# Kernel optimization log

Measured on AMD Instinct MI355X. Metric: run time of the kernel, lower is better.

## Reference

```python
import jax, jax.numpy as jnp
import numpy as np

O, I = 4096, 4096          # out_features, in_features
BLK = 32                   # GGML block size
NB = I // BLK              # blocks per output row
R = 16                     # LoRA rank
B, S = 8, 2048             # batch, seq
LORA_SCALE = 0.5           # alpha / rank
Q_ZERO = 128.0             # unsigned int storage -> signed via offset


def setup_inputs() -> dict:
    key = jax.random.key(0)
    k1, k2, k3, k4, k5, k6 = jax.random.split(key, 6)
    qweight = jax.random.randint(k1, (O, NB, BLK), 0, 256, dtype=jnp.int32)
    scales = jax.random.uniform(k2, (O, NB), dtype=jnp.float32) * 0.01
    lora_up = jax.random.normal(k3, (O, R), dtype=jnp.float32) * 0.02
    lora_down = jax.random.normal(k4, (R, I), dtype=jnp.float32) * 0.02
    bias = jax.random.normal(k5, (O,), dtype=jnp.float32)
    x = jax.random.normal(k6, (B, S, I), dtype=jnp.float32)
    return {"qweight": qweight, "scales": scales, "lora_up": lora_up,
            "lora_down": lora_down, "bias": bias, "x": x}


def reference(qweight, scales, lora_up, lora_down, bias, x):
    # GGML block dequantization: per-block scale times signed quantized values.
    deq = (scales[:, :, None] * (qweight.astype(jnp.float32) - Q_ZERO)).reshape(O, I)
    # LoRA-style patch applied to the dequantized weight.
    w = deq + LORA_SCALE * (lora_up @ lora_down)  # [O, I]
    # Fused use of the patched weight: linear layer.
    return jnp.einsum('bsi,oi->bso', x, w) + bias
```

## Files before the change

kernel.cpp:

```cpp
#include <hip/hip_runtime.h>
#include <stdint.h>

#define O_DIM 4096
#define I_DIM 4096
#define NB_DIM 128
#define R_DIM 16
#define M_DIM 16384
#define LORA_SCALE 0.5f
#define Q_ZERO 128.0f

typedef short bf16x8 __attribute__((ext_vector_type(8)));
typedef float f32x4 __attribute__((ext_vector_type(4)));

__device__ __forceinline__ uint16_t f2bf(float f) {
    union { float f; uint32_t u; } v; v.f = f;
    uint32_t u = v.u;
    return (uint16_t)((u + 0x7fffu + ((u >> 16) & 1u)) >> 16);
}

__device__ __forceinline__ void gll16(const void* g, void* l) {
    __builtin_amdgcn_global_load_lds(
        (const __attribute__((address_space(1))) void*)g,
        (__attribute__((address_space(3))) void*)l, 16, 0, 0);
}

__global__ void build_w_kernel(const int* __restrict__ qw,
                               const float* __restrict__ scales,
                               const float* __restrict__ up,
                               const float* __restrict__ down,
                               uint16_t* __restrict__ wout) {
    int idx = blockIdx.x * 256 + threadIdx.x;
    int i4  = idx & (I_DIM / 4 - 1);
    int o   = idx >> 10;
    int4 q = ((const int4*)qw)[(size_t)o * (I_DIM / 4) + i4];
    float scale = scales[o * NB_DIM + (i4 >> 3)];
    float a0 = 0.f, a1 = 0.f, a2 = 0.f, a3 = 0.f;
#pragma unroll
    for (int r = 0; r < R_DIM; ++r) {
        float u = up[o * R_DIM + r];
        float4 d = ((const float4*)down)[r * (I_DIM / 4) + i4];
        a0 += u * d.x; a1 += u * d.y; a2 += u * d.z; a3 += u * d.w;
    }
    float w0 = scale * ((float)q.x - Q_ZERO) + LORA_SCALE * a0;
    float w1 = scale * ((float)q.y - Q_ZERO) + LORA_SCALE * a1;
    float w2 = scale * ((float)q.z - Q_ZERO) + LORA_SCALE * a2;
    float w3 = scale * ((float)q.w - Q_ZERO) + LORA_SCALE * a3;
    ushort4 outv = { f2bf(w0), f2bf(w1), f2bf(w2), f2bf(w3) };
    ((ushort4*)wout)[(size_t)o * (I_DIM / 4) + i4] = outv;
}

__global__ void cvt_x_kernel(const float* __restrict__ x,
                             uint16_t* __restrict__ xb) {
    size_t idx = (size_t)blockIdx.x * 256 + threadIdx.x;
    float4 a = ((const float4*)x)[idx * 2];
    float4 b = ((const float4*)x)[idx * 2 + 1];
    ushort4 o0 = { f2bf(a.x), f2bf(a.y), f2bf(a.z), f2bf(a.w) };
    ushort4 o1 = { f2bf(b.x), f2bf(b.y), f2bf(b.z), f2bf(b.w) };
    ((ushort4*)xb)[idx * 2] = o0;
    ((ushort4*)xb)[idx * 2 + 1] = o1;
}

template <bool A_BF16>
__global__ void gemm_kernel(const uint16_t* __restrict__ Ab,
                            const float* __restrict__ Af,
                            const uint16_t* __restrict__ Wb,
                            const float* __restrict__ bias,
                            float* __restrict__ out) {
    __shared__ __align__(16) uint16_t As[128 * 32];
    __shared__ __align__(16) uint16_t Bs[128 * 32];
    const int tid = threadIdx.x;
    const int wave = tid >> 6, lane = tid & 63;
    const int m0 = blockIdx.y * 128;
    const int n0 = blockIdx.x * 128;
    const int wr = wave >> 1, wc = wave & 1;

    f32x4 acc[4][4] = {};

    const int lrow = lane & 15;
    const int lk = (lane >> 4) * 8;

    for (int k0 = 0; k0 < I_DIM; k0 += 32) {
        if (A_BF16) {
#pragma unroll
            for (int j = 0; j < 2; ++j) {
                int slot = wave * 2 + j;
                int row = slot * 16 + (lane >> 2);
                int col = (lane & 3) * 8;
                gll16(Ab + (size_t)(m0 + row) * I_DIM + k0 + col,
                      As + slot * 512);
            }
        } else {
            int row = tid >> 1;
            int col0 = (tid & 1) * 16;
            const float4* gp =
                (const float4*)(Af + (size_t)(m0 + row) * I_DIM + k0 + col0);
            float4 v0 = gp[0], v1 = gp[1], v2 = gp[2], v3 = gp[3];
            ushort4* dst = (ushort4*)&As[row * 32 + col0];
            ushort4 s0 = { f2bf(v0.x), f2bf(v0.y), f2bf(v0.z), f2bf(v0.w) };
            ushort4 s1 = { f2bf(v1.x), f2bf(v1.y), f2bf(v1.z), f2bf(v1.w) };
            ushort4 s2 = { f2bf(v2.x), f2bf(v2.y), f2bf(v2.z), f2bf(v2.w) };
            ushort4 s3 = { f2bf(v3.x), f2bf(v3.y), f2bf(v3.z), f2bf(v3.w) };
            dst[0] = s0; dst[1] = s1; dst[2] = s2; dst[3] = s3;
        }
#pragma unroll
        for (int j = 0; j < 2; ++j) {
            int slot = wave * 2 + j;
            int row = slot * 16 + (lane >> 2);
            int col = (lane & 3) * 8;
            gll16(Wb + (size_t)(n0 + row) * I_DIM + k0 + col,
                  Bs + slot * 512);
        }
        __syncthreads();

        bf16x8 a[4], b[4];
#pragma unroll
        for (int mi = 0; mi < 4; ++mi)
            a[mi] = *(const bf16x8*)&As[(wr * 64 + mi * 16 + lrow) * 32 + lk];
#pragma unroll
        for (int ni = 0; ni < 4; ++ni)
            b[ni] = *(const bf16x8*)&Bs[(wc * 64 + ni * 16 + lrow) * 32 + lk];
#pragma unroll
        for (int mi = 0; mi < 4; ++mi)
#pragma unroll
            for (int ni = 0; ni < 4; ++ni)
                acc[mi][ni] = __builtin_amdgcn_mfma_f32_16x16x32_bf16(
                    a[mi], b[ni], acc[mi][ni], 0, 0, 0);
        __syncthreads();
    }

    const int lcol = lane & 15;
    const int lquad = lane >> 4;
#pragma unroll
    for (int ni = 0; ni < 4; ++ni) {
        int n = n0 + wc * 64 + ni * 16 + lcol;
        float bv = bias[n];
#pragma unroll
        for (int mi = 0; mi < 4; ++mi) {
            int mbase = m0 + wr * 64 + mi * 16 + lquad * 4;
#pragma unroll
            for (int r = 0; r < 4; ++r)
                out[(size_t)(mbase + r) * O_DIM + n] = acc[mi][ni][r] + bv;
        }
    }
}

extern "C" void kernel_launch(void* const* d_in, const int* in_sizes, int n_in,
                              void* d_out, int out_size, void* d_ws,
                              size_t ws_size, hipStream_t stream) {
    const int* qweight = (const int*)d_in[0];
    const float* scales = (const float*)d_in[1];
    const float* lora_up = (const float*)d_in[2];
    const float* lora_down = (const float*)d_in[3];
    const float* bias = (const float*)d_in[4];
    const float* x = (const float*)d_in[5];
    float* out = (float*)d_out;

    uint16_t* w_bf16 = (uint16_t*)d_ws;
    const size_t w_bytes = (size_t)O_DIM * I_DIM * 2;
    uint16_t* x_bf16 = (uint16_t*)((char*)d_ws + w_bytes);
    const size_t need_full = w_bytes + (size_t)M_DIM * I_DIM * 2;

    build_w_kernel<<<O_DIM * I_DIM / 4 / 256, 256, 0, stream>>>(
        qweight, scales, lora_up, lora_down, w_bf16);

    dim3 grid(O_DIM / 128, M_DIM / 128);
    if (ws_size >= need_full) {
        cvt_x_kernel<<<(size_t)M_DIM * I_DIM / 8 / 256, 256, 0, stream>>>(
            x, x_bf16);
        gemm_kernel<true><<<grid, 256, 0, stream>>>(
            x_bf16, nullptr, w_bf16, bias, out);
    } else {
        gemm_kernel<false><<<grid, 256, 0, stream>>>(
            nullptr, x, w_bf16, bias, out);
    }
}
```

Baseline: 1.135 ms.

## Replace bf16 GEMM with 256x256-tile pipelined kernel using swizzled LDS and prefetch

Replaces the 128x128, single-buffered bf16 GEMM with a 512-thread kernel that computes 256x256 output tiles over K-steps of 64. LDS is double-buffered through direct global-to-LDS loads, with the next tiles' stages interleaved between MFMA groups and wait counts tuned for prefetch. LDS columns are XOR-swizzled to avoid bank conflicts, s_setprio is raised around the MFMA groups, and block IDs are remapped for L2 locality. The aim is more operand reuse per tile, overlap of loads with compute, and fewer stalls. The costs are 128KB of LDS per block, higher register pressure from 128 accumulators, and many barriers per iteration.

```diff
diff --git a/kernel.cpp b/kernel.cpp
--- a/kernel.cpp
+++ b/kernel.cpp
@@ -6,6 +6,7 @@
 #define NB_DIM 128
 #define R_DIM 16
 #define M_DIM 16384
+#define NT_K 64
 #define LORA_SCALE 0.5f
 #define Q_ZERO 128.0f
 
@@ -60,12 +61,10 @@
     ((ushort4*)xb)[idx * 2 + 1] = o1;
 }
 
-template <bool A_BF16>
-__global__ void gemm_kernel(const uint16_t* __restrict__ Ab,
-                            const float* __restrict__ Af,
-                            const uint16_t* __restrict__ Wb,
-                            const float* __restrict__ bias,
-                            float* __restrict__ out) {
+__global__ void gemm_kernel_f32a(const float* __restrict__ Af,
+                                 const uint16_t* __restrict__ Wb,
+                                 const float* __restrict__ bias,
+                                 float* __restrict__ out) {
     __shared__ __align__(16) uint16_t As[128 * 32];
     __shared__ __align__(16) uint16_t Bs[128 * 32];
     const int tid = threadIdx.x;
@@ -75,21 +74,11 @@
     const int wr = wave >> 1, wc = wave & 1;
 
     f32x4 acc[4][4] = {};
-
     const int lrow = lane & 15;
     const int lk = (lane >> 4) * 8;
 
     for (int k0 = 0; k0 < I_DIM; k0 += 32) {
-        if (A_BF16) {
-#pragma unroll
-            for (int j = 0; j < 2; ++j) {
-                int slot = wave * 2 + j;
-                int row = slot * 16 + (lane >> 2);
-                int col = (lane & 3) * 8;
-                gll16(Ab + (size_t)(m0 + row) * I_DIM + k0 + col,
-                      As + slot * 512);
-            }
-        } else {
+        {
             int row = tid >> 1;
             int col0 = (tid & 1) * 16;
             const float4* gp =
@@ -111,7 +100,6 @@
                   Bs + slot * 512);
         }
         __syncthreads();
-
         bf16x8 a[4], b[4];
 #pragma unroll
         for (int mi = 0; mi < 4; ++mi)
@@ -142,6 +130,140 @@
                 out[(size_t)(mbase + r) * O_DIM + n] = acc[mi][ni][r] + bv;
         }
     }
+}
+
+__global__ __launch_bounds__(512, 2)
+void gemm256_kernel(const uint16_t* __restrict__ Ab,
+                    const uint16_t* __restrict__ Wb,
+                    const float* __restrict__ bias,
+                    float* __restrict__ out) {
+    __shared__ __align__(16) char smem[131072];
+    const int tid = threadIdx.x;
+    const int wave = tid >> 6;
+    const int lane = tid & 63;
+
+    int bid = blockIdx.x;
+    int swz = (bid & 7) * 128 + (bid >> 3);
+    const int tn = swz >> 6;
+    const int tm = swz & 63;
+    const int m0 = tm * 256;
+    const int n0 = tn * 256;
+
+    const int wr = wave >> 2;
+    const int wc = wave & 3;
+
+    const int srow = lane >> 3;
+    const int sslot = (lane & 7) ^ srow;
+
+    const int l15 = lane & 15, q = lane >> 4, l7 = lane & 7;
+    const int ps0 = ((q ^ l7) << 4);
+    const int ps1 = (((4 | q) ^ l7) << 4);
+    const int abase = wr * 16384 + l15 * 128;
+    const int bbase = 65536 + (wc >> 1) * 16384 + ((wc & 1) * 64 + l15) * 128;
+
+    f32x4 acc[8][4] = {};
+    bf16x8 a[8][2], b[2][2];
+
+#define STAGE_HALF(mat, row0, kt, ldsb)                                       \
+    {                                                                         \
+        _Pragma("unroll")                                                     \
+        for (int j = 0; j < 2; ++j) {                                         \
+            const uint16_t* g = (mat) +                                       \
+                (size_t)((row0) + j * 64 + wave * 8 + srow) * I_DIM +         \
+                (size_t)(kt) * 64 + sslot * 8;                                \
+            gll16(g, smem + (ldsb) + (j * 64 + wave * 8) * 128);              \
+        }                                                                     \
+    }
+
+#define LDA(co, mi) do {                                                      \
+        a[mi][0] = *(const bf16x8*)(smem + (co) + abase + (mi) * 2048 + ps0); \
+        a[mi][1] = *(const bf16x8*)(smem + (co) + abase + (mi) * 2048 + ps1); \
+    } while (0)
+
+#define LDB(co, bi, nn) do {                                                  \
+        b[bi][0] = *(const bf16x8*)(smem + (co) + bbase + (nn) * 2048 + ps0); \
+        b[bi][1] = *(const bf16x8*)(smem + (co) + bbase + (nn) * 2048 + ps1); \
+    } while (0)
+
+#define MFMA_QUAD(MI0, NI0)                                                   \
+    _Pragma("unroll")                                                         \
+    for (int mi = 0; mi < 4; ++mi)                                            \
+        _Pragma("unroll")                                                     \
+        for (int ni = 0; ni < 2; ++ni)                                        \
+            _Pragma("unroll")                                                 \
+            for (int kk = 0; kk < 2; ++kk)                                    \
+                acc[(MI0) + mi][(NI0) + ni] =                                 \
+                    __builtin_amdgcn_mfma_f32_16x16x32_bf16(                  \
+                        a[(MI0) + mi][kk], b[ni][kk],                         \
+                        acc[(MI0) + mi][(NI0) + ni], 0, 0, 0);
+
+    STAGE_HALF(Ab, m0,       0, 0);
+    STAGE_HALF(Ab, m0 + 128, 0, 16384);
+    STAGE_HALF(Wb, n0,       0, 65536);
+    STAGE_HALF(Wb, n0 + 128, 0, 65536 + 16384);
+    STAGE_HALF(Ab, m0,       1, 32768);
+    STAGE_HALF(Ab, m0 + 128, 1, 32768 + 16384);
+    asm volatile("s_waitcnt vmcnt(4)" ::: "memory");
+    __builtin_amdgcn_s_barrier();
+
+#pragma unroll 2
+    for (int t = 0; t < NT_K; ++t) {
+        const int co = (t & 1) * 32768;
+        const int po = co ^ 32768;
+#pragma unroll
+        for (int mi = 0; mi < 4; ++mi) LDA(co, mi);
+        LDB(co, 0, 0); LDB(co, 1, 1);
+        if (t + 1 < NT_K) STAGE_HALF(Wb, n0, t + 1, 65536 + po);
+        __builtin_amdgcn_s_barrier();
+        __builtin_amdgcn_s_setprio(1);
+        MFMA_QUAD(0, 0)
+        __builtin_amdgcn_s_setprio(0);
+        __builtin_amdgcn_s_barrier();
+#pragma unroll
+        for (int mi = 0; mi < 4; ++mi) LDA(co, 4 + mi);
+        if (t + 1 < NT_K) STAGE_HALF(Wb, n0 + 128, t + 1, 65536 + po + 16384);
+        __builtin_amdgcn_s_barrier();
+        __builtin_amdgcn_s_setprio(1);
+        MFMA_QUAD(4, 0)
+        __builtin_amdgcn_s_setprio(0);
+        __builtin_amdgcn_s_barrier();
+        LDB(co, 0, 2); LDB(co, 1, 3);
+        if (t + 2 < NT_K) STAGE_HALF(Ab, m0, t + 2, co);
+        __builtin_amdgcn_s_barrier();
+        __builtin_amdgcn_s_setprio(1);
+        MFMA_QUAD(4, 2)
+        __builtin_amdgcn_s_setprio(0);
+        __builtin_amdgcn_s_barrier();
+        if (t + 2 < NT_K) STAGE_HALF(Ab, m0 + 128, t + 2, co + 16384);
+        __builtin_amdgcn_s_barrier();
+        __builtin_amdgcn_s_setprio(1);
+        MFMA_QUAD(0, 2)
+        __builtin_amdgcn_s_setprio(0);
+        if (t < NT_K - 2) {
+            asm volatile("s_waitcnt vmcnt(4)" ::: "memory");
+        } else {
+            asm volatile("s_waitcnt vmcnt(0)" ::: "memory");
+        }
+        __builtin_amdgcn_s_barrier();
+    }
+
+    const int lq = lane >> 4;
+#pragma unroll
+    for (int ni = 0; ni < 4; ++ni) {
+        int n = n0 + wc * 64 + ni * 16 + l15;
+        float bv = bias[n];
+#pragma unroll
+        for (int mi = 0; mi < 8; ++mi) {
+            int mbase = m0 + wr * 128 + mi * 16 + lq * 4;
+#pragma unroll
+            for (int r = 0; r < 4; ++r)
+                out[(size_t)(mbase + r) * O_DIM + n] = acc[mi][ni][r] + bv;
+        }
+    }
+#undef STAGE_HALF
+#undef LDA
+#undef LDB
+#undef MFMA_QUAD
 }
 
 extern "C" void kernel_launch(void* const* d_in, const int* in_sizes, int n_in,
@@ -163,14 +285,13 @@
     build_w_kernel<<<O_DIM * I_DIM / 4 / 256, 256, 0, stream>>>(
         qweight, scales, lora_up, lora_down, w_bf16);
 
-    dim3 grid(O_DIM / 128, M_DIM / 128);
     if (ws_size >= need_full) {
         cvt_x_kernel<<<(size_t)M_DIM * I_DIM / 8 / 256, 256, 0, stream>>>(
             x, x_bf16);
-        gemm_kernel<true><<<grid, 256, 0, stream>>>(
-            x_bf16, nullptr, w_bf16, bias, out);
+        gemm256_kernel<<<dim3((M_DIM / 256) * (O_DIM / 256)), 512, 0, stream>>>(
+            x_bf16, w_bf16, bias, out);
     } else {
-        gemm_kernel<false><<<grid, 256, 0, stream>>>(
-            nullptr, x, w_bf16, bias, out);
-    }
-}
+        dim3 grid(O_DIM / 128, M_DIM / 128);
+        gemm_kernel_f32a<<<grid, 256, 0, stream>>>(x, w_bf16, bias, out);
+    }
+}
```

Measured after the change: 972.4 us. 14.3% less time.
